# Performance work log

Measured on AMD Instinct MI355X. Metric: run time of the kernel, lower is better.

## Reference

```python
import jax, jax.numpy as jnp
import numpy as np

N_NODES = 100000
N_EDGES = 800000
IN_C, HID_C, OUT_C = 128, 64, 40


def setup_inputs() -> dict:
    key = jax.random.key(0)
    k1, k2, k3, k4, k5, k6 = jax.random.split(key, 6)
    x = jax.random.normal(k1, (N_NODES, IN_C), dtype=jnp.float32)
    edge_index = jax.random.randint(k2, (2, N_EDGES), 0, N_NODES, dtype=jnp.int64)
    W1 = jax.random.normal(k3, (IN_C, HID_C), dtype=jnp.float32) * (1.0 / np.sqrt(IN_C))
    b1 = jax.random.normal(k4, (HID_C,), dtype=jnp.float32) * 0.01
    W2 = jax.random.normal(k5, (HID_C, OUT_C), dtype=jnp.float32) * (1.0 / np.sqrt(HID_C))
    b2 = jax.random.normal(k6, (OUT_C,), dtype=jnp.float32) * 0.01
    return {"x": x, "edge_index": edge_index, "W1": W1, "b1": b1, "W2": W2, "b2": b2}


def _sg_propagate(x, src, dst, n):
    # GCN symmetric normalization (self-loops already appended by caller):
    # deg[i] = number of incoming edges at i; norm_e = deg[src]^-1/2 * deg[dst]^-1/2
    deg = jax.ops.segment_sum(jnp.ones_like(dst, dtype=x.dtype), dst, num_segments=n)
    dinv = jnp.where(deg > 0, jax.lax.rsqrt(deg), jnp.zeros_like(deg))
    norm = dinv[src] * dinv[dst]  # [E]
    # out[i] = sum_{e: dst_e=i} norm_e * x[src_e]
    return jax.ops.segment_sum(x[src] * norm[:, None], dst, num_segments=n)


def reference(x, edge_index, W1, b1, W2, b2):
    n = x.shape[0]
    loop = jnp.arange(n, dtype=edge_index.dtype)
    src = jnp.concatenate([edge_index[0], loop])
    dst = jnp.concatenate([edge_index[1], loop])
    # dropout is identity in eval mode
    h = _sg_propagate(x, src, dst, n) @ W1 + b1   # SGConv(in_c, hid_c), K=1
    h = jax.nn.relu(h)
    o = _sg_propagate(h, src, dst, n) @ W2 + b2   # SGConv(hid_c, out_c), K=1
    return jax.nn.log_softmax(o, axis=1)
```

## Files before the change

kernel.cpp:

```cpp
#include <hip/hip_runtime.h>
#include <math.h>

#define IN_C 128
#define HID_C 64
#define OUT_C 40

__global__ void zero4_kernel(int4* __restrict__ p, long long n4) {
  long long i = (long long)blockIdx.x * blockDim.x + threadIdx.x;
  long long stride = (long long)gridDim.x * blockDim.x;
  for (; i < n4; i += stride) p[i] = make_int4(0, 0, 0, 0);
}

__global__ void degpos_kernel(const int* __restrict__ dst, int E,
                              int* __restrict__ deg, int* __restrict__ pos) {
  int base = blockIdx.x * blockDim.x + threadIdx.x;
  int stride = gridDim.x * blockDim.x;
  for (int e = base; e < E; e += 4 * stride) {
    int e1 = e + stride, e2 = e + 2 * stride, e3 = e + 3 * stride;
    bool g1 = e1 < E, g2 = e2 < E, g3 = e3 < E;
    int d0 = dst[e];
    int d1 = g1 ? dst[e1] : 0;
    int d2 = g2 ? dst[e2] : 0;
    int d3 = g3 ? dst[e3] : 0;
    int p0 = atomicAdd(&deg[d0], 1);
    int p1 = g1 ? atomicAdd(&deg[d1], 1) : 0;
    int p2 = g2 ? atomicAdd(&deg[d2], 1) : 0;
    int p3 = g3 ? atomicAdd(&deg[d3], 1) : 0;
    pos[e] = p0;
    if (g1) pos[e1] = p1;
    if (g2) pos[e2] = p2;
    if (g3) pos[e3] = p3;
  }
}

__global__ __launch_bounds__(256) void scan1_kernel(
    const int* __restrict__ deg, int* __restrict__ S, int* __restrict__ BS,
    int n) {
  __shared__ int sums[256];
  int t = threadIdx.x;
  int i0 = blockIdx.x * 1024 + t * 4;
  int v0 = (i0 + 0 < n) ? deg[i0 + 0] : 0;
  int v1 = (i0 + 1 < n) ? deg[i0 + 1] : 0;
  int v2 = (i0 + 2 < n) ? deg[i0 + 2] : 0;
  int v3 = (i0 + 3 < n) ? deg[i0 + 3] : 0;
  v1 += v0; v2 += v1; v3 += v2;
  sums[t] = v3;
  __syncthreads();
  for (int off = 1; off < 256; off <<= 1) {
    int x = (t >= off) ? sums[t - off] : 0;
    __syncthreads();
    sums[t] += x;
    __syncthreads();
  }
  int excl = t ? sums[t - 1] : 0;
  if (i0 + 0 < n) S[i0 + 0] = v0 + excl;
  if (i0 + 1 < n) S[i0 + 1] = v1 + excl;
  if (i0 + 2 < n) S[i0 + 2] = v2 + excl;
  if (i0 + 3 < n) S[i0 + 3] = v3 + excl;
  if (t == 255) BS[blockIdx.x] = sums[255];
}

__global__ __launch_bounds__(128) void scan2_kernel(int* __restrict__ BS,
                                                    int nb) {
  __shared__ int s[128];
  int t = threadIdx.x;
  s[t] = (t < nb) ? BS[t] : 0;
  __syncthreads();
  for (int off = 1; off < 128; off <<= 1) {
    int x = (t >= off) ? s[t - off] : 0;
    __syncthreads();
    s[t] += x;
    __syncthreads();
  }
  if (t < nb) BS[t] = t ? s[t - 1] : 0;
}

__global__ void scan3_kernel(const int* __restrict__ S,
                             const int* __restrict__ BS,
                             const int* __restrict__ deg,
                             int* __restrict__ rowptr,
                             float* __restrict__ dinv, int n) {
  int i = blockIdx.x * blockDim.x + threadIdx.x;
  if (i < n) {
    int d = deg[i];
    int r = S[i] + BS[i >> 10];
    rowptr[i + 1] = r;
    dinv[i] = rsqrtf((float)d + 1.0f);
    if (i == 0) rowptr[0] = 0;
  }
}

#define XS_LD 68
#define FILL_BLOCKS 1024
__global__ __launch_bounds__(256) void fused_fill_gemm1_kernel(
    const int* __restrict__ eidx, int E, const int* __restrict__ rowptr,
    const int* __restrict__ pos, int* __restrict__ csr,
    const float* __restrict__ x, const float* __restrict__ W1,
    const float* __restrict__ dinv, float* __restrict__ y, int n) {
  __shared__ float xs[64 * XS_LD];
  __shared__ float wsh[64 * HID_C];
  int t = threadIdx.x;
  if ((int)blockIdx.x < FILL_BLOCKS) {
    int base = blockIdx.x * 256 + t;
    int stride = FILL_BLOCKS * 256;
    for (int e = base; e < E; e += 4 * stride) {
      int e1 = e + stride, e2 = e + 2 * stride, e3 = e + 3 * stride;
      bool g1 = e1 < E, g2 = e2 < E, g3 = e3 < E;
      int s0 = eidx[e], d0 = eidx[E + e], p0 = pos[e];
      int s1 = 0, d1 = 0, p1 = 0, s2 = 0, d2 = 0, p2 = 0, s3 = 0, d3 = 0, p3 = 0;
      if (g1) { s1 = eidx[e1]; d1 = eidx[E + e1]; p1 = pos[e1]; }
      if (g2) { s2 = eidx[e2]; d2 = eidx[E + e2]; p2 = pos[e2]; }
      if (g3) { s3 = eidx[e3]; d3 = eidx[E + e3]; p3 = pos[e3]; }
      int r0 = rowptr[d0];
      int r1 = g1 ? rowptr[d1] : 0;
      int r2 = g2 ? rowptr[d2] : 0;
      int r3 = g3 ? rowptr[d3] : 0;
      csr[r0 + p0] = s0;
      if (g1) csr[r1 + p1] = s1;
      if (g2) csr[r2 + p2] = s2;
      if (g3) csr[r3 + p3] = s3;
    }
    return;
  }
  int rowBase = ((int)blockIdx.x - FILL_BLOCKS) * 64;
  const float4* xf4 = (const float4*)x;
  const float4* wf4 = (const float4*)W1;
  int tx = t & 15, ty = t >> 4;
  int i0 = ty * 4, j0 = tx * 4;
  float acc[4][4];
#pragma unroll
  for (int r = 0; r < 4; ++r)
#pragma unroll
    for (int j = 0; j < 4; ++j) acc[r][j] = 0.f;

  for (int kc = 0; kc < 2; ++kc) {
#pragma unroll
    for (int k = 0; k < 4; ++k) {
      int t4 = t + k * 256;
      int row = t4 >> 4, c4 = t4 & 15;
      int gr = rowBase + row;
      if (gr >= n) gr = n - 1;
      *(float4*)&xs[row * XS_LD + c4 * 4] = xf4[(size_t)gr * 32 + kc * 16 + c4];
      *(float4*)&wsh[row * HID_C + c4 * 4] = wf4[(size_t)(kc * 64 + row) * 16 + c4];
    }
    __syncthreads();
#pragma unroll 2
    for (int c4 = 0; c4 < 64; c4 += 4) {
      float4 xv[4], wv[4];
#pragma unroll
      for (int r = 0; r < 4; ++r)
        xv[r] = *(const float4*)&xs[(i0 + r) * XS_LD + c4];
#pragma unroll
      for (int cc = 0; cc < 4; ++cc)
        wv[cc] = *(const float4*)&wsh[(c4 + cc) * HID_C + j0];
#pragma unroll
      for (int r = 0; r < 4; ++r) {
#pragma unroll
        for (int cc = 0; cc < 4; ++cc) {
          float xr = (&xv[r].x)[cc];
          acc[r][0] = fmaf(xr, wv[cc].x, acc[r][0]);
          acc[r][1] = fmaf(xr, wv[cc].y, acc[r][1]);
          acc[r][2] = fmaf(xr, wv[cc].z, acc[r][2]);
          acc[r][3] = fmaf(xr, wv[cc].w, acc[r][3]);
        }
      }
    }
    __syncthreads();
  }
#pragma unroll
  for (int r = 0; r < 4; ++r) {
    int i = rowBase + i0 + r;
    if (i < n) {
      float di = dinv[i];
      float4 v = make_float4(di * acc[r][0], di * acc[r][1],
                             di * acc[r][2], di * acc[r][3]);
      *(float4*)&y[(size_t)i * HID_C + j0] = v;
    }
  }
}

__global__ __launch_bounds__(256) void gather1_kernel(
    const float4* __restrict__ y4, const int* __restrict__ rowptr,
    const int* __restrict__ csr, const float* __restrict__ dinv,
    const float* __restrict__ b1, float* __restrict__ h, int n) {
  int lane = threadIdx.x & 63;
  int grp = lane >> 4;
  int q = lane & 15;
  float4 b1v = ((const float4*)b1)[q];
  int wid = (int)((blockIdx.x * blockDim.x + threadIdx.x) >> 6);
  int nw = (int)((gridDim.x * blockDim.x) >> 6);
  int ii = wid;
  int e0 = 0, e1 = 0; float di = 0.f;
  if (ii < n) { e0 = rowptr[ii]; e1 = rowptr[ii + 1]; di = dinv[ii]; }
  while (ii < n) {
    int nxt = ii + nw;
    int ne0 = 0, ne1 = 0; float ndi = 0.f;
    if (nxt < n) { ne0 = rowptr[nxt]; ne1 = rowptr[nxt + 1]; ndi = dinv[nxt]; }
    int i = __builtin_amdgcn_readfirstlane(ii);
    float4 acc = make_float4(0.f, 0.f, 0.f, 0.f);
    if (grp == 0) acc = y4[(size_t)i * 16 + q];
    int e = e0 + grp, end = e1;
    for (; e + 4 < end; e += 8) {
      int s0 = csr[e], s1 = csr[e + 4];
      float4 v0 = y4[(size_t)s0 * 16 + q];
      float4 v1 = y4[(size_t)s1 * 16 + q];
      acc.x += v0.x + v1.x;
      acc.y += v0.y + v1.y;
      acc.z += v0.z + v1.z;
      acc.w += v0.w + v1.w;
    }
    for (; e < end; e += 4) {
      int s = csr[e];
      float4 v = y4[(size_t)s * 16 + q];
      acc.x += v.x; acc.y += v.y; acc.z += v.z; acc.w += v.w;
    }
    acc.x += __shfl_xor(acc.x, 16); acc.y += __shfl_xor(acc.y, 16);
    acc.z += __shfl_xor(acc.z, 16); acc.w += __shfl_xor(acc.w, 16);
    acc.x += __shfl_xor(acc.x, 32); acc.y += __shfl_xor(acc.y, 32);
    acc.z += __shfl_xor(acc.z, 32); acc.w += __shfl_xor(acc.w, 32);
    if (grp == 0) {
      float4 hv;
      hv.x = fmaf(di, acc.x, b1v.x); hv.x = hv.x > 0.f ? hv.x : 0.f;
      hv.y = fmaf(di, acc.y, b1v.y); hv.y = hv.y > 0.f ? hv.y : 0.f;
      hv.z = fmaf(di, acc.z, b1v.z); hv.z = hv.z > 0.f ? hv.z : 0.f;
      hv.w = fmaf(di, acc.w, b1v.w); hv.w = hv.w > 0.f ? hv.w : 0.f;
      *(float4*)&h[(size_t)i * HID_C + 4 * q] = hv;
    }
    ii = nxt; e0 = ne0; e1 = ne1; di = ndi;
  }
}

__global__ __launch_bounds__(256) void gemm2_kernel(
    const float* __restrict__ h, const float* __restrict__ W2,
    const float* __restrict__ dinv, float* __restrict__ z, int n) {
  __shared__ float hs[64 * XS_LD];
  __shared__ float w2s[64 * OUT_C + 32];
  int t = threadIdx.x;
  int rowBase = blockIdx.x * 64;
  const float4* hf4 = (const float4*)h;
  const float4* wf4 = (const float4*)W2;
#pragma unroll
  for (int k = 0; k < 4; ++k) {
    int t4 = t + k * 256;
    int row = t4 >> 4, c4 = t4 & 15;
    int gr = rowBase + row;
    if (gr >= n) gr = n - 1;
    *(float4*)&hs[row * XS_LD + c4 * 4] = hf4[(size_t)gr * 16 + c4];
  }
  for (int t4 = t; t4 < 640; t4 += 256)
    *(float4*)&w2s[t4 * 4] = wf4[t4];
  __syncthreads();
  int tx = t & 15, ty = t >> 4;
  int i0 = ty * 4, j0 = tx * 4;
  bool active = tx < 10;
  float acc[4][4];
#pragma unroll
  for (int r = 0; r < 4; ++r)
#pragma unroll
    for (int j = 0; j < 4; ++j) acc[r][j] = 0.f;
#pragma unroll 2
  for (int c4 = 0; c4 < 64; c4 += 4) {
    float4 hv[4], wv[4];
#pragma unroll
    for (int r = 0; r < 4; ++r)
      hv[r] = *(const float4*)&hs[(i0 + r) * XS_LD + c4];
#pragma unroll
    for (int cc = 0; cc < 4; ++cc)
      wv[cc] = *(const float4*)&w2s[(c4 + cc) * OUT_C + j0];
#pragma unroll
    for (int r = 0; r < 4; ++r) {
#pragma unroll
      for (int cc = 0; cc < 4; ++cc) {
        float hr = (&hv[r].x)[cc];
        acc[r][0] = fmaf(hr, wv[cc].x, acc[r][0]);
        acc[r][1] = fmaf(hr, wv[cc].y, acc[r][1]);
        acc[r][2] = fmaf(hr, wv[cc].z, acc[r][2]);
        acc[r][3] = fmaf(hr, wv[cc].w, acc[r][3]);
      }
    }
  }
  if (active) {
#pragma unroll
    for (int r = 0; r < 4; ++r) {
      int i = rowBase + i0 + r;
      if (i < n) {
        float di = dinv[i];
        float4 v = make_float4(di * acc[r][0], di * acc[r][1],
                               di * acc[r][2], di * acc[r][3]);
        *(float4*)&z[(size_t)i * OUT_C + j0] = v;
      }
    }
  }
}

__global__ __launch_bounds__(256) void gather40_kernel(
    const float4* __restrict__ z4, const int* __restrict__ rowptr,
    const int* __restrict__ csr, const float* __restrict__ dinv,
    const float* __restrict__ b2, float* __restrict__ out, int n) {
  int lane = threadIdx.x & 63;
  int grp = lane >> 4;
  int q = lane & 15;
  bool act = q < 10;
  float4 b2v = ((const float4*)b2)[act ? q : 0];
  int wid = (int)((blockIdx.x * blockDim.x + threadIdx.x) >> 6);
  int nw = (int)((gridDim.x * blockDim.x) >> 6);
  int ii = wid;
  int e0 = 0, e1 = 0; float di = 0.f;
  if (ii < n) { e0 = rowptr[ii]; e1 = rowptr[ii + 1]; di = dinv[ii]; }
  while (ii < n) {
    int nxt = ii + nw;
    int ne0 = 0, ne1 = 0; float ndi = 0.f;
    if (nxt < n) { ne0 = rowptr[nxt]; ne1 = rowptr[nxt + 1]; ndi = dinv[nxt]; }
    int i = __builtin_amdgcn_readfirstlane(ii);
    float4 acc = make_float4(0.f, 0.f, 0.f, 0.f);
    if (grp == 0 && act) acc = z4[(size_t)i * 10 + q];
    int e = e0 + grp, end = e1;
    if (act) {
      for (; e + 4 < end; e += 8) {
        int s0 = csr[e], s1 = csr[e + 4];
        float4 v0 = z4[(size_t)s0 * 10 + q];
        float4 v1 = z4[(size_t)s1 * 10 + q];
        acc.x += v0.x + v1.x;
        acc.y += v0.y + v1.y;
        acc.z += v0.z + v1.z;
        acc.w += v0.w + v1.w;
      }
      for (; e < end; e += 4) {
        int s = csr[e];
        float4 v = z4[(size_t)s * 10 + q];
        acc.x += v.x; acc.y += v.y; acc.z += v.z; acc.w += v.w;
      }
    }
    acc.x += __shfl_xor(acc.x, 16); acc.y += __shfl_xor(acc.y, 16);
    acc.z += __shfl_xor(acc.z, 16); acc.w += __shfl_xor(acc.w, 16);
    acc.x += __shfl_xor(acc.x, 32); acc.y += __shfl_xor(acc.y, 32);
    acc.z += __shfl_xor(acc.z, 32); acc.w += __shfl_xor(acc.w, 32);
    float4 o;
    o.x = fmaf(di, acc.x, b2v.x);
    o.y = fmaf(di, acc.y, b2v.y);
    o.z = fmaf(di, acc.z, b2v.z);
    o.w = fmaf(di, acc.w, b2v.w);
    float m = act ? fmaxf(fmaxf(o.x, o.y), fmaxf(o.z, o.w)) : -INFINITY;
    for (int off = 8; off; off >>= 1) m = fmaxf(m, __shfl_xor(m, off));
    float ex = act ? (expf(o.x - m) + expf(o.y - m) +
                      expf(o.z - m) + expf(o.w - m)) : 0.f;
    float s = ex;
    for (int off = 8; off; off >>= 1) s += __shfl_xor(s, off);
    if (lane < 16 && act) {
      float l = m + logf(s);
      float4 o2 = make_float4(o.x - l, o.y - l, o.z - l, o.w - l);
      *(float4*)&out[(size_t)i * OUT_C + 4 * q] = o2;
    }
    ii = nxt; e0 = ne0; e1 = ne1; di = ndi;
  }
}

extern "C" void kernel_launch(void* const* d_in, const int* in_sizes, int n_in,
                              void* d_out, int out_size, void* d_ws, size_t ws_size,
                              hipStream_t stream) {
  const float* x  = (const float*)d_in[0];
  const int* eidx = (const int*)d_in[1];
  const float* W1 = (const float*)d_in[2];
  const float* b1 = (const float*)d_in[3];
  const float* W2 = (const float*)d_in[4];
  const float* b2 = (const float*)d_in[5];
  float* out = (float*)d_out;

  int n = in_sizes[0] / IN_C;
  int E = in_sizes[1] / 2;

  size_t npad = ((size_t)n + 255) & ~(size_t)255;
  size_t Epad = ((size_t)E + 255) & ~(size_t)255;
  size_t o_dinv   = 0;
  size_t o_deg    = o_dinv + npad;
  size_t o_S      = o_deg + npad;
  size_t o_BS     = o_S + npad;
  size_t o_rowptr = o_BS + 256;
  size_t o_pos    = o_rowptr + npad + 256;
  size_t o_csr    = o_pos + Epad;
  size_t o_bufA   = o_csr + Epad;
  size_t o_bufC   = o_bufA + (size_t)n * HID_C;
  size_t needed   = (o_bufC + (size_t)n * HID_C) * 4;
  if (ws_size < needed) return;

  float* ws  = (float*)d_ws;
  float* dinv = ws + o_dinv;
  int* deg    = (int*)(ws + o_deg);
  int* S      = (int*)(ws + o_S);
  int* BS     = (int*)(ws + o_BS);
  int* rowptr = (int*)(ws + o_rowptr);
  int* pos    = (int*)(ws + o_pos);
  int* csr    = (int*)(ws + o_csr);
  float* bufA = ws + o_bufA;
  float* bufC = ws + o_bufC;

  int nb = (int)((n + 1023) / 1024);

  zero4_kernel<<<128, 256, 0, stream>>>((int4*)deg, (long long)(npad / 4));
  degpos_kernel<<<1024, 256, 0, stream>>>(eidx + E, E, deg, pos);
  scan1_kernel<<<nb, 256, 0, stream>>>(deg, S, BS, n);
  scan2_kernel<<<1, 128, 0, stream>>>(BS, nb);
  scan3_kernel<<<(n + 255) / 256, 256, 0, stream>>>(S, BS, deg, rowptr, dinv, n);

  int gemmBlocks = (n + 63) / 64;
  fused_fill_gemm1_kernel<<<FILL_BLOCKS + gemmBlocks, 256, 0, stream>>>(
      eidx, E, rowptr, pos, csr, x, W1, dinv, bufA, n);

  gather1_kernel<<<2048, 256, 0, stream>>>((const float4*)bufA, rowptr, csr,
                                           dinv, b1, bufC, n);
  gemm2_kernel<<<(n + 63) / 64, 256, 0, stream>>>(bufC, W2, dinv, bufA, n);
  gather40_kernel<<<2048, 256, 0, stream>>>((const float4*)bufA, rowptr, csr,
                                            dinv, b2, out, n);
}
```

Measured before the change: 182.0 us.

## Overlap degree counting with GEMM1 and defer dinv scaling to fill kernel

GEMM1 (x@W1) now runs in the same launch as the degree/position atomic pass, since it no longer needs dinv; the dinv row scaling moves into a separate elementwise pass fused with the CSR fill kernel. The aim is to hide the GEMM's compute and x read behind the latency-bound atomic histogram. The cost is an extra read-modify-write pass over the n x 64 intermediate buffer.

```diff
diff --git a/kernel.cpp b/kernel.cpp
--- a/kernel.cpp
+++ b/kernel.cpp
@@ -9,28 +9,6 @@
   long long i = (long long)blockIdx.x * blockDim.x + threadIdx.x;
   long long stride = (long long)gridDim.x * blockDim.x;
   for (; i < n4; i += stride) p[i] = make_int4(0, 0, 0, 0);
-}
-
-__global__ void degpos_kernel(const int* __restrict__ dst, int E,
-                              int* __restrict__ deg, int* __restrict__ pos) {
-  int base = blockIdx.x * blockDim.x + threadIdx.x;
-  int stride = gridDim.x * blockDim.x;
-  for (int e = base; e < E; e += 4 * stride) {
-    int e1 = e + stride, e2 = e + 2 * stride, e3 = e + 3 * stride;
-    bool g1 = e1 < E, g2 = e2 < E, g3 = e3 < E;
-    int d0 = dst[e];
-    int d1 = g1 ? dst[e1] : 0;
-    int d2 = g2 ? dst[e2] : 0;
-    int d3 = g3 ? dst[e3] : 0;
-    int p0 = atomicAdd(&deg[d0], 1);
-    int p1 = g1 ? atomicAdd(&deg[d1], 1) : 0;
-    int p2 = g2 ? atomicAdd(&deg[d2], 1) : 0;
-    int p3 = g3 ? atomicAdd(&deg[d3], 1) : 0;
-    pos[e] = p0;
-    if (g1) pos[e1] = p1;
-    if (g2) pos[e2] = p2;
-    if (g3) pos[e3] = p3;
-  }
 }
 
 __global__ __launch_bounds__(256) void scan1_kernel(
@@ -91,18 +69,100 @@
 }
 
 #define XS_LD 68
-#define FILL_BLOCKS 1024
-__global__ __launch_bounds__(256) void fused_fill_gemm1_kernel(
-    const int* __restrict__ eidx, int E, const int* __restrict__ rowptr,
-    const int* __restrict__ pos, int* __restrict__ csr,
-    const float* __restrict__ x, const float* __restrict__ W1,
-    const float* __restrict__ dinv, float* __restrict__ y, int n) {
+#define DP_BLOCKS 1024
+__global__ __launch_bounds__(256) void fused_degpos_gemm1_kernel(
+    const int* __restrict__ dst, int E, int* __restrict__ deg,
+    int* __restrict__ pos, const float* __restrict__ x,
+    const float* __restrict__ W1, float* __restrict__ y, int n) {
   __shared__ float xs[64 * XS_LD];
   __shared__ float wsh[64 * HID_C];
   int t = threadIdx.x;
-  if ((int)blockIdx.x < FILL_BLOCKS) {
+  if ((int)blockIdx.x < DP_BLOCKS) {
     int base = blockIdx.x * 256 + t;
-    int stride = FILL_BLOCKS * 256;
+    int stride = DP_BLOCKS * 256;
+    for (int e = base; e < E; e += 4 * stride) {
+      int e1 = e + stride, e2 = e + 2 * stride, e3 = e + 3 * stride;
+      bool g1 = e1 < E, g2 = e2 < E, g3 = e3 < E;
+      int d0 = dst[e];
+      int d1 = g1 ? dst[e1] : 0;
+      int d2 = g2 ? dst[e2] : 0;
+      int d3 = g3 ? dst[e3] : 0;
+      int p0 = atomicAdd(&deg[d0], 1);
+      int p1 = g1 ? atomicAdd(&deg[d1], 1) : 0;
+      int p2 = g2 ? atomicAdd(&deg[d2], 1) : 0;
+      int p3 = g3 ? atomicAdd(&deg[d3], 1) : 0;
+      pos[e] = p0;
+      if (g1) pos[e1] = p1;
+      if (g2) pos[e2] = p2;
+      if (g3) pos[e3] = p3;
+    }
+    return;
+  }
+  int rowBase = ((int)blockIdx.x - DP_BLOCKS) * 64;
+  const float4* xf4 = (const float4*)x;
+  const float4* wf4 = (const float4*)W1;
+  int tx = t & 15, ty = t >> 4;
+  int i0 = ty * 4, j0 = tx * 4;
+  float acc[4][4];
+#pragma unroll
+  for (int r = 0; r < 4; ++r)
+#pragma unroll
+    for (int j = 0; j < 4; ++j) acc[r][j] = 0.f;
+
+  for (int kc = 0; kc < 2; ++kc) {
+#pragma unroll
+    for (int k = 0; k < 4; ++k) {
+      int t4 = t + k * 256;
+      int row = t4 >> 4, c4 = t4 & 15;
+      int gr = rowBase + row;
+      if (gr >= n) gr = n - 1;
+      *(float4*)&xs[row * XS_LD + c4 * 4] = xf4[(size_t)gr * 32 + kc * 16 + c4];
+      *(float4*)&wsh[row * HID_C + c4 * 4] = wf4[(size_t)(kc * 64 + row) * 16 + c4];
+    }
+    __syncthreads();
+#pragma unroll 2
+    for (int c4 = 0; c4 < 64; c4 += 4) {
+      float4 xv[4], wv[4];
+#pragma unroll
+      for (int r = 0; r < 4; ++r)
+        xv[r] = *(const float4*)&xs[(i0 + r) * XS_LD + c4];
+#pragma unroll
+      for (int cc = 0; cc < 4; ++cc)
+        wv[cc] = *(const float4*)&wsh[(c4 + cc) * HID_C + j0];
+#pragma unroll
+      for (int r = 0; r < 4; ++r) {
+#pragma unroll
+        for (int cc = 0; cc < 4; ++cc) {
+          float xr = (&xv[r].x)[cc];
+          acc[r][0] = fmaf(xr, wv[cc].x, acc[r][0]);
+          acc[r][1] = fmaf(xr, wv[cc].y, acc[r][1]);
+          acc[r][2] = fmaf(xr, wv[cc].z, acc[r][2]);
+          acc[r][3] = fmaf(xr, wv[cc].w, acc[r][3]);
+        }
+      }
+    }
+    __syncthreads();
+  }
+#pragma unroll
+  for (int r = 0; r < 4; ++r) {
+    int i = rowBase + i0 + r;
+    if (i < n) {
+      float4 v = make_float4(acc[r][0], acc[r][1], acc[r][2], acc[r][3]);
+      *(float4*)&y[(size_t)i * HID_C + j0] = v;
+    }
+  }
+}
+
+#define FB_BLOCKS 1024
+#define SC_BLOCKS 1024
+__global__ __launch_bounds__(256) void fused_fill_scale_kernel(
+    const int* __restrict__ eidx, int E, const int* __restrict__ rowptr,
+    const int* __restrict__ pos, int* __restrict__ csr,
+    const float* __restrict__ dinv, float4* __restrict__ y4, int n) {
+  int t = threadIdx.x;
+  if ((int)blockIdx.x < FB_BLOCKS) {
+    int base = blockIdx.x * 256 + t;
+    int stride = FB_BLOCKS * 256;
     for (int e = base; e < E; e += 4 * stride) {
       int e1 = e + stride, e2 = e + 2 * stride, e3 = e + 3 * stride;
       bool g1 = e1 < E, g2 = e2 < E, g3 = e3 < E;
@@ -122,60 +182,14 @@
     }
     return;
   }
-  int rowBase = ((int)blockIdx.x - FILL_BLOCKS) * 64;
-  const float4* xf4 = (const float4*)x;
-  const float4* wf4 = (const float4*)W1;
-  int tx = t & 15, ty = t >> 4;
-  int i0 = ty * 4, j0 = tx * 4;
-  float acc[4][4];
-#pragma unroll
-  for (int r = 0; r < 4; ++r)
-#pragma unroll
-    for (int j = 0; j < 4; ++j) acc[r][j] = 0.f;
-
-  for (int kc = 0; kc < 2; ++kc) {
-#pragma unroll
-    for (int k = 0; k < 4; ++k) {
-      int t4 = t + k * 256;
-      int row = t4 >> 4, c4 = t4 & 15;
-      int gr = rowBase + row;
-      if (gr >= n) gr = n - 1;
-      *(float4*)&xs[row * XS_LD + c4 * 4] = xf4[(size_t)gr * 32 + kc * 16 + c4];
-      *(float4*)&wsh[row * HID_C + c4 * 4] = wf4[(size_t)(kc * 64 + row) * 16 + c4];
-    }
-    __syncthreads();
-#pragma unroll 2
-    for (int c4 = 0; c4 < 64; c4 += 4) {
-      float4 xv[4], wv[4];
-#pragma unroll
-      for (int r = 0; r < 4; ++r)
-        xv[r] = *(const float4*)&xs[(i0 + r) * XS_LD + c4];
-#pragma unroll
-      for (int cc = 0; cc < 4; ++cc)
-        wv[cc] = *(const float4*)&wsh[(c4 + cc) * HID_C + j0];
-#pragma unroll
-      for (int r = 0; r < 4; ++r) {
-#pragma unroll
-        for (int cc = 0; cc < 4; ++cc) {
-          float xr = (&xv[r].x)[cc];
-          acc[r][0] = fmaf(xr, wv[cc].x, acc[r][0]);
-          acc[r][1] = fmaf(xr, wv[cc].y, acc[r][1]);
-          acc[r][2] = fmaf(xr, wv[cc].z, acc[r][2]);
-          acc[r][3] = fmaf(xr, wv[cc].w, acc[r][3]);
-        }
-      }
-    }
-    __syncthreads();
-  }
-#pragma unroll
-  for (int r = 0; r < 4; ++r) {
-    int i = rowBase + i0 + r;
-    if (i < n) {
-      float di = dinv[i];
-      float4 v = make_float4(di * acc[r][0], di * acc[r][1],
-                             di * acc[r][2], di * acc[r][3]);
-      *(float4*)&y[(size_t)i * HID_C + j0] = v;
-    }
+  long long total = (long long)n * 16;
+  long long base = (long long)((int)blockIdx.x - FB_BLOCKS) * 256 + t;
+  long long stride = (long long)SC_BLOCKS * 256;
+  for (long long idx = base; idx < total; idx += stride) {
+    int i = (int)(idx >> 4);
+    float di = dinv[i];
+    float4 v = y4[idx];
+    y4[idx] = make_float4(di * v.x, di * v.y, di * v.z, di * v.w);
   }
 }
 
@@ -395,20 +409,22 @@
   float* bufC = ws + o_bufC;
 
   int nb = (int)((n + 1023) / 1024);
+  int gemmBlocks = (n + 63) / 64;
 
   zero4_kernel<<<128, 256, 0, stream>>>((int4*)deg, (long long)(npad / 4));
-  degpos_kernel<<<1024, 256, 0, stream>>>(eidx + E, E, deg, pos);
+  fused_degpos_gemm1_kernel<<<DP_BLOCKS + gemmBlocks, 256, 0, stream>>>(
+      eidx + E, E, deg, pos, x, W1, bufA, n);
+
   scan1_kernel<<<nb, 256, 0, stream>>>(deg, S, BS, n);
   scan2_kernel<<<1, 128, 0, stream>>>(BS, nb);
   scan3_kernel<<<(n + 255) / 256, 256, 0, stream>>>(S, BS, deg, rowptr, dinv, n);
 
-  int gemmBlocks = (n + 63) / 64;
-  fused_fill_gemm1_kernel<<<FILL_BLOCKS + gemmBlocks, 256, 0, stream>>>(
-      eidx, E, rowptr, pos, csr, x, W1, dinv, bufA, n);
+  fused_fill_scale_kernel<<<FB_BLOCKS + SC_BLOCKS, 256, 0, stream>>>(
+      eidx, E, rowptr, pos, csr, dinv, (float4*)bufA, n);
 
   gather1_kernel<<<2048, 256, 0, stream>>>((const float4*)bufA, rowptr, csr,
                                            dinv, b1, bufC, n);
-  gemm2_kernel<<<(n + 63) / 64, 256, 0, stream>>>(bufC, W2, dinv, bufA, n);
+  gemm2_kernel<<<gemmBlocks, 256, 0, stream>>>(bufC, W2, dinv, bufA, n);
   gather40_kernel<<<2048, 256, 0, stream>>>((const float4*)bufA, rowptr, csr,
                                             dinv, b2, out, n);
 }
```

Measured after the change: 189.8 us. +4.3%, slower.
